# Performance work log

Measured on AMD Instinct MI355X. Metric: run time of the kernel, lower is better.

## Reference

```python
import jax, jax.numpy as jnp
import numpy as np

DELTA = 5.0          # weight on positive BCE term
R = 0.01             # hard-negative fraction
M, N = 4096, 16384   # batch rows, memory-bank size
NUM_HARD = int(R * (N - 1))  # int(r * neg_count); each row has exactly 1 positive


def setup_inputs() -> dict:
    key = jax.random.key(0)
    k1, k2 = jax.random.split(key)
    inputs = jax.random.normal(k1, (M, N), dtype=jnp.float32)
    targets = jax.random.randint(k2, (M,), 0, N)
    return {"inputs": inputs, "targets": targets}


def reference(inputs, targets):
    m, n = inputs.shape
    rows = jnp.arange(m)
    # positive logit per row (one-hot scatter => exactly one positive)
    pos = inputs[rows, targets]                          # [m]
    # BCE with logits, target=1: softplus(-x); mean over the single positive
    l_pos = jax.nn.softplus(-pos)                        # [m]
    # exclude positive from negatives by sinking it to -inf, then hard top-k
    neg_inf = jnp.finfo(inputs.dtype).min
    masked = inputs.at[rows, targets].set(neg_inf)       # [m, n]
    hard_neg, _ = jax.lax.top_k(masked, NUM_HARD)        # [m, NUM_HARD]
    # BCE with logits, target=0: softplus(x); mean over hard negatives
    l_neg = jnp.mean(jax.nn.softplus(hard_neg), axis=1)  # [m]
    return jnp.mean(DELTA * l_pos + l_neg)
```

## Files before the change

kernel.cpp:

```cpp
#include <hip/hip_runtime.h>
#include <stdint.h>

#define M_ROWS 4096
#define N_COLS 16384
#define K_HARD 163
#define DELTA_W 5.0f
#define BLOCK  256
#define THRESH 2.0f
#define KEY_MIN 0xC0000000u
#define SEGG   192
#define CAP    1536
#define NB     1024
#define SMALL  64
#define SLOTA  13

__device__ __forceinline__ uint32_t f2key(float x) {
    uint32_t u = __float_as_uint(x);
    return u ^ (uint32_t)(((int32_t)u >> 31) | 0x80000000u);
}
__device__ __forceinline__ float key2f(uint32_t k) {
    uint32_t u = (k & 0x80000000u) ? (k & 0x7fffffffu) : ~k;
    return __uint_as_float(u);
}
__device__ __forceinline__ float softplus_f(float x) {
    return fmaxf(x, 0.0f) + log1pf(__expf(-fabsf(x)));
}

__device__ void pivot_scan(const uint32_t* hist, int K,
                           int* part, int* pivot, int* krem) {
    const int t = threadIdx.x;
    const int bpt = NB / BLOCK;
    const int base = t * bpt;
    int mypart = 0;
    for (int i = 0; i < bpt; ++i) mypart += (int)hist[base + i];
    part[t] = mypart;
    __syncthreads();
    for (int off = 1; off < BLOCK; off <<= 1) {
        int v = part[t];
        if (t + off < BLOCK) v += part[t + off];
        __syncthreads();
        part[t] = v;
        __syncthreads();
    }
    const int above = part[t] - mypart;
    if (above < K && above + mypart >= K) {
        int running = above;
        for (int b = base + bpt - 1; b >= base; --b) {
            int c = (int)hist[b];
            if (running < K && running + c >= K) { *pivot = b; *krem = K - running; }
            running += c;
        }
    }
    __syncthreads();
}

__global__ __launch_bounds__(BLOCK) void k1_filter(
        const float* __restrict__ inputs,
        uint32_t* __restrict__ counts,
        float4* __restrict__ groups) {
    const int row = blockIdx.x;
    const int lane = threadIdx.x & 63;
    const int wid = threadIdx.x >> 6;
    const float4* rp4 = (const float4*)(inputs + (size_t)row * N_COLS);
    float4* seg = groups + (size_t)(row * 4 + wid) * SEGG;
    uint32_t wcount = 0;
#pragma unroll 4
    for (int it = 0; it < N_COLS / (BLOCK * 4); ++it) {
        const float4 v = rp4[wid * 1024 + it * 64 + lane];
        const float m = fmaxf(fmaxf(v.x, v.y), fmaxf(v.z, v.w));
        const bool pred = (m >= THRESH);
        const unsigned long long mask = __ballot(pred);
        if (pred) {
            const int below = __builtin_amdgcn_mbcnt_hi(
                (uint32_t)(mask >> 32),
                __builtin_amdgcn_mbcnt_lo((uint32_t)mask, 0));
            const uint32_t off = wcount + (uint32_t)below;
            if (off < SEGG) seg[off] = v;
        }
        wcount += (uint32_t)__popcll(mask);
    }
    if (lane == 0) counts[row * 4 + wid] = wcount;
}

__global__ __launch_bounds__(BLOCK) void k2_select(
        const float* __restrict__ inputs,
        const int* __restrict__ targets,
        const uint32_t* __restrict__ counts,
        const float4* __restrict__ groups,
        float* __restrict__ out) {
    __shared__ float    s_slots_f[BLOCK * SLOTA];
    __shared__ uint32_t s_cand[CAP];
    __shared__ int s_wc[4], s_wt[4];
    __shared__ int s_found, s_pivot, s_krem, s_nsmall;
    __shared__ uint32_t s_skey[SMALL];
    __shared__ int s_sidx[SMALL];
    __shared__ float s_fw[4];

    const int row = blockIdx.x;
    const int t = threadIdx.x;
    const int lane = t & 63;
    const int wid = t >> 6;
    const float* rowp = inputs + (size_t)row * N_COLS;
    const int target = targets[row];

    if (t == 0) s_found = -1;
    if (t < 4) s_wc[t] = (int)counts[row * 4 + t];
    __syncthreads();
    const int cw0 = s_wc[0], cw1 = s_wc[1], cw2 = s_wc[2], cw3 = s_wc[3];
    const bool ovf = (cw0 > SEGG) | (cw1 > SEGG) | (cw2 > SEGG) | (cw3 > SEGG);

    float* myslots = s_slots_f + t * SLOTA;
    uint32_t c = 0;
    if (!ovf) {
        const int cw = s_wc[wid];
        const float4* seg = groups + (size_t)(row * 4 + wid) * SEGG;
#pragma unroll
        for (int g = 0; g < SEGG / 64; ++g) {
            const int gi = g * 64 + lane;
            if (gi < cw) {
                const float4 v = seg[gi];
                myslots[min(c, (uint32_t)(SLOTA - 1))] = v.x; c += (v.x >= THRESH);
                myslots[min(c, (uint32_t)(SLOTA - 1))] = v.y; c += (v.y >= THRESH);
                myslots[min(c, (uint32_t)(SLOTA - 1))] = v.z; c += (v.z >= THRESH);
                myslots[min(c, (uint32_t)(SLOTA - 1))] = v.w; c += (v.w >= THRESH);
            }
        }
    }

    const int stored = (int)c;
    int inc = stored;
    for (int off = 1; off < 64; off <<= 1) {
        int y = __shfl_up(inc, off);
        if (lane >= off) inc += y;
    }
    if (lane == 63) s_wt[wid] = inc;
    __syncthreads();
    const int w0 = s_wt[0], w1 = s_wt[1], w2 = s_wt[2], w3 = s_wt[3];
    const int total = w0 + w1 + w2 + w3;
    const int wbase = (wid > 0 ? w0 : 0) + (wid > 1 ? w1 : 0) + (wid > 2 ? w2 : 0);
    const int myoff = wbase + inc - stored;
    for (int j = 0; j < stored; ++j) {
        const int d = myoff + j;
        if (d < CAP) s_cand[d] = f2key(myslots[j]);
    }
    __syncthreads();

    const float pos = rowp[target];
    const uint32_t tkey = f2key(pos);
    const int tclamp = min(total, CAP);
    if (pos >= THRESH) {
        for (int i = t; i < tclamp; i += BLOCK)
            if (s_cand[i] == tkey) { atomicCAS(&s_found, -1, i); break; }
    }
    __syncthreads();
    int ncand = total;
    if (s_found >= 0) {
        ncand = total - 1;
        if (t == 0) s_cand[s_found] = s_cand[ncand];
    }
    __syncthreads();

    const bool fast = !ovf && (total <= CAP) && (ncand >= K_HARD);
    bool needfb = !fast;
    float local = 0.0f;
    uint32_t* hist = (uint32_t*)s_slots_f;

    if (fast) {
        for (int i = t; i < NB; i += BLOCK) hist[i] = 0;
        __syncthreads();
        for (int i = t; i < ncand; i += BLOCK)
            atomicAdd(&hist[min((s_cand[i] - KEY_MIN) >> 14, (uint32_t)(NB - 1))], 1u);
        __syncthreads();

        const int base4 = t * 4;
        const int c0 = (int)hist[base4], c1 = (int)hist[base4 + 1],
                  c2 = (int)hist[base4 + 2], c3 = (int)hist[base4 + 3];
        const int own = c0 + c1 + c2 + c3;
        int suf = own;
        for (int off = 1; off < 64; off <<= 1) {
            int y = __shfl_down(suf, off);
            if (lane + off < 64) suf += y;
        }
        if (lane == 0) s_wt[wid] = suf;
        if (t == 0) s_nsmall = 0;
        __syncthreads();
        int wsuf = 0;
        for (int w = wid + 1; w < 4; ++w) wsuf += s_wt[w];
        int run = wsuf + (suf - own);
        {
            const int cs[4] = {c0, c1, c2, c3};
            for (int b = 3; b >= 0; --b) {
                const int cc = cs[b];
                if (run < K_HARD && run + cc >= K_HARD) {
                    s_pivot = base4 + b; s_krem = K_HARD - run;
                }
                run += cc;
            }
        }
        __syncthreads();
        const uint32_t B = (uint32_t)s_pivot;
        const int krem = s_krem;

        for (int i = t; i < ncand; i += BLOCK) {
            const uint32_t k = s_cand[i];
            const uint32_t kb = min((k - KEY_MIN) >> 14, (uint32_t)(NB - 1));
            if (kb > B) local += softplus_f(key2f(k));
            else if (kb == B) {
                const int d = atomicAdd(&s_nsmall, 1);
                if (d < SMALL) { s_skey[d] = k; s_sidx[d] = i; }
            }
        }
        __syncthreads();
        const int m = s_nsmall;
        if (m > SMALL) { needfb = true; local = 0.0f; }
        else {
            for (int i = t; i < m; i += BLOCK) {
                const uint32_t ki = s_skey[i]; const int ii = s_sidx[i];
                int r = 0;
                for (int j = 0; j < m; ++j) {
                    const uint32_t kj = s_skey[j];
                    r += (kj > ki) || (kj == ki && s_sidx[j] < ii);
                }
                if (r < krem) local += softplus_f(key2f(ki));
            }
        }
    }

    if (needfb) {
        local = 0.0f;
        int* part = (int*)s_cand;
        for (int i = t; i < NB; i += BLOCK) hist[i] = 0;
        __syncthreads();
        for (int j = t; j < N_COLS; j += BLOCK) {
            if (j == target) continue;
            atomicAdd(&hist[f2key(rowp[j]) >> 22], 1u);
        }
        __syncthreads();
        pivot_scan(hist, K_HARD, part, &s_pivot, &s_krem);
        const int p1 = s_pivot, k1r = s_krem;

        for (int i = t; i < NB; i += BLOCK) hist[i] = 0;
        __syncthreads();
        for (int j = t; j < N_COLS; j += BLOCK) {
            if (j == target) continue;
            const uint32_t k = f2key(rowp[j]);
            if ((int)(k >> 22) == p1) atomicAdd(&hist[(k >> 12) & 1023u], 1u);
        }
        __syncthreads();
        pivot_scan(hist, k1r, part, &s_pivot, &s_krem);
        const uint32_t pref2 = ((uint32_t)p1 << 10) | (uint32_t)s_pivot;
        const int k2r = s_krem;

        for (int i = t; i < NB; i += BLOCK) hist[i] = 0;
        __syncthreads();
        for (int j = t; j < N_COLS; j += BLOCK) {
            if (j == target) continue;
            const uint32_t k = f2key(rowp[j]);
            if ((k >> 12) == pref2) atomicAdd(&hist[(k >> 2) & 1023u], 1u);
        }
        __syncthreads();
        pivot_scan(hist, k2r, part, &s_pivot, &s_krem);
        const uint32_t pref3 = (pref2 << 10) | (uint32_t)s_pivot;
        const int k3r = s_krem;

        for (int i = t; i < 4; i += BLOCK) hist[i] = 0;
        __syncthreads();
        for (int j = t; j < N_COLS; j += BLOCK) {
            if (j == target) continue;
            const uint32_t k = f2key(rowp[j]);
            if ((k >> 2) == pref3) atomicAdd(&hist[k & 3u], 1u);
        }
        __syncthreads();
        if (t == 0) {
            int running = 0;
            for (int b = 3; b >= 0; --b) {
                const int cc = (int)hist[b];
                if (running < k3r && running + cc >= k3r) {
                    s_pivot = b; s_krem = k3r - running;
                }
                running += cc;
            }
        }
        __syncthreads();
        const uint32_t T = (pref3 << 2) | (uint32_t)s_pivot;
        const int tie = s_krem;

        for (int j = t; j < N_COLS; j += BLOCK) {
            if (j == target) continue;
            const uint32_t k = f2key(rowp[j]);
            if (k > T) local += softplus_f(key2f(k));
        }
        if (t == 0) local += (float)tie * softplus_f(key2f(T));
    }

    for (int off = 32; off > 0; off >>= 1) local += __shfl_down(local, off);
    if (lane == 0) s_fw[wid] = local;
    __syncthreads();
    if (t == 0) {
        const float tot = s_fw[0] + s_fw[1] + s_fw[2] + s_fw[3];
        const float l_neg = tot / (float)K_HARD;
        const float l_pos = softplus_f(-pos);
        const float rowval = (DELTA_W * l_pos + l_neg) * (1.0f / (float)M_ROWS);
        atomicAdd(out, rowval);
    }
}

__global__ void mmcl_zero_out(float* out) { out[0] = 0.0f; }

extern "C" void kernel_launch(void* const* d_in, const int* in_sizes, int n_in,
                              void* d_out, int out_size, void* d_ws, size_t ws_size,
                              hipStream_t stream) {
    const float* inputs = (const float*)d_in[0];
    const int* targets = (const int*)d_in[1];
    float* out = (float*)d_out;
    uint32_t* counts = (uint32_t*)d_ws;
    float4* groups = (float4*)((char*)d_ws + 65536);
    mmcl_zero_out<<<1, 1, 0, stream>>>(out);
    k1_filter<<<M_ROWS, BLOCK, 0, stream>>>(inputs, counts, groups);
    k2_select<<<M_ROWS, BLOCK, 0, stream>>>(inputs, targets, counts, groups, out);
}
```

Baseline: 417.2 us.

## Fuse filter and select kernels, keep candidate groups in shared memory

Merges the filter kernel and the selection kernel into one per-row kernel, so the candidate float4 groups go to LDS instead of a global workspace and are not re-read from global memory. Candidates are compacted in two passes over the LDS segments (count, then write), replacing the per-thread slot array. The global atomicAdd into the output is replaced by per-row partial results and a single-block reduce kernel, which also removes the zero-init launch. Shared memory per block changes from the slot array to 12KB of segments, which could affect occupancy.

```diff
diff --git a/kernel.cpp b/kernel.cpp
--- a/kernel.cpp
+++ b/kernel.cpp
@@ -12,7 +12,6 @@
 #define CAP    1536
 #define NB     1024
 #define SMALL  64
-#define SLOTA  13
 
 __device__ __forceinline__ uint32_t f2key(float x) {
     uint32_t u = __float_as_uint(x);
@@ -54,18 +53,32 @@
     __syncthreads();
 }
 
-__global__ __launch_bounds__(BLOCK) void k1_filter(
+__global__ __launch_bounds__(BLOCK) void mmcl_main(
         const float* __restrict__ inputs,
-        uint32_t* __restrict__ counts,
-        float4* __restrict__ groups) {
+        const int* __restrict__ targets,
+        float* __restrict__ partial) {
+    __shared__ float4   s_seg[4 * SEGG];
+    __shared__ uint32_t s_cand[CAP];
+    __shared__ int s_wt[4], s_wc[4];
+    __shared__ int s_found, s_pivot, s_krem, s_nsmall;
+    __shared__ uint32_t s_skey[SMALL];
+    __shared__ int s_sidx[SMALL];
+    __shared__ float s_fw[4];
+
     const int row = blockIdx.x;
-    const int lane = threadIdx.x & 63;
-    const int wid = threadIdx.x >> 6;
-    const float4* rp4 = (const float4*)(inputs + (size_t)row * N_COLS);
-    float4* seg = groups + (size_t)(row * 4 + wid) * SEGG;
+    const int t = threadIdx.x;
+    const int lane = t & 63;
+    const int wid = t >> 6;
+    const float* rowp = inputs + (size_t)row * N_COLS;
+    const int target = targets[row];
+
+    if (t == 0) s_found = -1;
+
+    float4* wseg = s_seg + wid * SEGG;
     uint32_t wcount = 0;
+    const float4* rp4 = (const float4*)rowp;
 #pragma unroll 4
-    for (int it = 0; it < N_COLS / (BLOCK * 4); ++it) {
+    for (int it = 0; it < 16; ++it) {
         const float4 v = rp4[wid * 1024 + it * 64 + lane];
         const float m = fmaxf(fmaxf(v.x, v.y), fmaxf(v.z, v.w));
         const bool pred = (m >= THRESH);
@@ -75,60 +88,23 @@
                 (uint32_t)(mask >> 32),
                 __builtin_amdgcn_mbcnt_lo((uint32_t)mask, 0));
             const uint32_t off = wcount + (uint32_t)below;
-            if (off < SEGG) seg[off] = v;
+            if (off < SEGG) wseg[off] = v;
         }
         wcount += (uint32_t)__popcll(mask);
     }
-    if (lane == 0) counts[row * 4 + wid] = wcount;
-}
-
-__global__ __launch_bounds__(BLOCK) void k2_select(
-        const float* __restrict__ inputs,
-        const int* __restrict__ targets,
-        const uint32_t* __restrict__ counts,
-        const float4* __restrict__ groups,
-        float* __restrict__ out) {
-    __shared__ float    s_slots_f[BLOCK * SLOTA];
-    __shared__ uint32_t s_cand[CAP];
-    __shared__ int s_wc[4], s_wt[4];
-    __shared__ int s_found, s_pivot, s_krem, s_nsmall;
-    __shared__ uint32_t s_skey[SMALL];
-    __shared__ int s_sidx[SMALL];
-    __shared__ float s_fw[4];
-
-    const int row = blockIdx.x;
-    const int t = threadIdx.x;
-    const int lane = t & 63;
-    const int wid = t >> 6;
-    const float* rowp = inputs + (size_t)row * N_COLS;
-    const int target = targets[row];
-
-    if (t == 0) s_found = -1;
-    if (t < 4) s_wc[t] = (int)counts[row * 4 + t];
-    __syncthreads();
-    const int cw0 = s_wc[0], cw1 = s_wc[1], cw2 = s_wc[2], cw3 = s_wc[3];
-    const bool ovf = (cw0 > SEGG) | (cw1 > SEGG) | (cw2 > SEGG) | (cw3 > SEGG);
-
-    float* myslots = s_slots_f + t * SLOTA;
-    uint32_t c = 0;
-    if (!ovf) {
-        const int cw = s_wc[wid];
-        const float4* seg = groups + (size_t)(row * 4 + wid) * SEGG;
+    if (lane == 0) s_wc[wid] = (int)wcount;
+
+    const int cwg = (int)min(wcount, (uint32_t)SEGG);
+    int cnt = 0;
 #pragma unroll
-        for (int g = 0; g < SEGG / 64; ++g) {
-            const int gi = g * 64 + lane;
-            if (gi < cw) {
-                const float4 v = seg[gi];
-                myslots[min(c, (uint32_t)(SLOTA - 1))] = v.x; c += (v.x >= THRESH);
-                myslots[min(c, (uint32_t)(SLOTA - 1))] = v.y; c += (v.y >= THRESH);
-                myslots[min(c, (uint32_t)(SLOTA - 1))] = v.z; c += (v.z >= THRESH);
-                myslots[min(c, (uint32_t)(SLOTA - 1))] = v.w; c += (v.w >= THRESH);
-            }
-        }
-    }
-
-    const int stored = (int)c;
-    int inc = stored;
+    for (int g = 0; g < 3; ++g) {
+        const int gi = g * 64 + lane;
+        if (gi < cwg) {
+            const float4 v = wseg[gi];
+            cnt += (v.x >= THRESH) + (v.y >= THRESH) + (v.z >= THRESH) + (v.w >= THRESH);
+        }
+    }
+    int inc = cnt;
     for (int off = 1; off < 64; off <<= 1) {
         int y = __shfl_up(inc, off);
         if (lane >= off) inc += y;
@@ -137,11 +113,28 @@
     __syncthreads();
     const int w0 = s_wt[0], w1 = s_wt[1], w2 = s_wt[2], w3 = s_wt[3];
     const int total = w0 + w1 + w2 + w3;
+    const bool ovf = (s_wc[0] > SEGG) | (s_wc[1] > SEGG) |
+                     (s_wc[2] > SEGG) | (s_wc[3] > SEGG);
     const int wbase = (wid > 0 ? w0 : 0) + (wid > 1 ? w1 : 0) + (wid > 2 ? w2 : 0);
-    const int myoff = wbase + inc - stored;
-    for (int j = 0; j < stored; ++j) {
-        const int d = myoff + j;
-        if (d < CAP) s_cand[d] = f2key(myslots[j]);
+    const int myoff = wbase + inc - cnt;
+
+    {
+        int c = 0;
+        for (int g = 0; g < 3; ++g) {
+            const int gi = g * 64 + lane;
+            if (gi < cwg) {
+                const float4 v = wseg[gi];
+                const float e[4] = {v.x, v.y, v.z, v.w};
+#pragma unroll
+                for (int q = 0; q < 4; ++q) {
+                    if (e[q] >= THRESH) {
+                        const int d = myoff + c;
+                        if (d < CAP) s_cand[d] = f2key(e[q]);
+                        ++c;
+                    }
+                }
+            }
+        }
     }
     __syncthreads();
 
@@ -163,7 +156,7 @@
     const bool fast = !ovf && (total <= CAP) && (ncand >= K_HARD);
     bool needfb = !fast;
     float local = 0.0f;
-    uint32_t* hist = (uint32_t*)s_slots_f;
+    uint32_t* hist = (uint32_t*)s_seg;
 
     if (fast) {
         for (int i = t; i < NB; i += BLOCK) hist[i] = 0;
@@ -300,12 +293,22 @@
         const float tot = s_fw[0] + s_fw[1] + s_fw[2] + s_fw[3];
         const float l_neg = tot / (float)K_HARD;
         const float l_pos = softplus_f(-pos);
-        const float rowval = (DELTA_W * l_pos + l_neg) * (1.0f / (float)M_ROWS);
-        atomicAdd(out, rowval);
-    }
-}
-
-__global__ void mmcl_zero_out(float* out) { out[0] = 0.0f; }
+        partial[row] = DELTA_W * l_pos + l_neg;
+    }
+}
+
+__global__ __launch_bounds__(BLOCK) void mmcl_reduce(
+        const float* __restrict__ partial, float* __restrict__ out) {
+    __shared__ float s_fw[4];
+    const int t = threadIdx.x;
+    float local = 0.0f;
+    for (int i = t; i < M_ROWS; i += BLOCK) local += partial[i];
+    for (int off = 32; off > 0; off >>= 1) local += __shfl_down(local, off);
+    if ((t & 63) == 0) s_fw[t >> 6] = local;
+    __syncthreads();
+    if (t == 0)
+        out[0] = (s_fw[0] + s_fw[1] + s_fw[2] + s_fw[3]) * (1.0f / (float)M_ROWS);
+}
 
 extern "C" void kernel_launch(void* const* d_in, const int* in_sizes, int n_in,
                               void* d_out, int out_size, void* d_ws, size_t ws_size,
@@ -313,9 +316,7 @@
     const float* inputs = (const float*)d_in[0];
     const int* targets = (const int*)d_in[1];
     float* out = (float*)d_out;
-    uint32_t* counts = (uint32_t*)d_ws;
-    float4* groups = (float4*)((char*)d_ws + 65536);
-    mmcl_zero_out<<<1, 1, 0, stream>>>(out);
-    k1_filter<<<M_ROWS, BLOCK, 0, stream>>>(inputs, counts, groups);
-    k2_select<<<M_ROWS, BLOCK, 0, stream>>>(inputs, targets, counts, groups, out);
-}
+    float* partial = (float*)d_ws;
+    mmcl_main<<<M_ROWS, BLOCK, 0, stream>>>(inputs, targets, partial);
+    mmcl_reduce<<<1, BLOCK, 0, stream>>>(partial, out);
+}
```

Result: faster. 364.6 us (-12.6%).
